# Optimization experiments

Measured on AMD Instinct MI355X. Metric: run time of the kernel, lower is better.

Reference implementation:

```python
import jax, jax.numpy as jnp
import numpy as np

GROUP_SIZE = 128


def setup_inputs() -> dict:
    key = jax.random.key(0)
    k1, k2, k3, k4, k5 = jax.random.split(key, 5)
    B, S, I, O = 4, 2048, 4096, 4096
    x = jax.random.normal(k1, (B, S, I), dtype=jnp.float32)
    logits = jax.random.normal(k2, (O, I, 3), dtype=jnp.float32)
    u = jax.random.uniform(k3, (O, I, 3), dtype=jnp.float32)
    scales = jax.random.uniform(k4, (O, I // GROUP_SIZE), dtype=jnp.float32)
    mask = jax.random.randint(k5, (O, I), 0, 2, dtype=jnp.int32)
    return {"x": x, "logits": logits, "u": u, "scales": scales, "mask": mask}


def reference(x, logits, u, scales, mask):
    # Gumbel noise: E ~ Exp(1) via inverse CDF, gumbel = -log(max(E, 1e-10))
    e = -jnp.log(jnp.clip(1.0 - u, 1e-12, 1.0))
    gumbels = -jnp.log(jnp.clip(e, 1e-10, None))
    # hard ternary sample (training path of TernaryReinMax.forward)
    samples = jnp.argmax(logits + gumbels, axis=-1)          # [O, I]
    one_hot = jax.nn.one_hot(samples, 3, dtype=jnp.float32)   # [O, I, 3]
    w = one_hot[..., 2] - one_hot[..., 0]                     # ternary {-1,0,1}
    O, I = w.shape
    G = GROUP_SIZE
    # per-group dequant scales along in_features, then mask
    w = (w.reshape(O, I // G, G) * scales[:, :, None]).reshape(O, I)
    w = w * mask.astype(w.dtype)
    # F.linear(x, w) = x @ w.T
    return jnp.einsum('bsi,oi->bso', x, w.astype(x.dtype))
```

## Files before the change

kernel.cpp:

```cpp
#include <hip/hip_runtime.h>
#include <hip/hip_bf16.h>

typedef unsigned short ushort_t;
typedef __attribute__((ext_vector_type(4))) float f32x4;
typedef __attribute__((ext_vector_type(8))) short short8;
typedef __attribute__((ext_vector_type(4))) unsigned short u16x4;
typedef __attribute__((ext_vector_type(8))) unsigned short u16x8;
typedef __attribute__((ext_vector_type(4))) int i32x4;

constexpr int Mdim = 8192;
constexpr int Ndim = 4096;
constexpr int Kdim = 4096;
constexpr int BM = 128, BN = 128, BK = 32;

__device__ __forceinline__ ushort_t f2bf(float f) {
  unsigned u = __float_as_uint(f);
  u += 0x7fffu + ((u >> 16) & 1u);
  return (ushort_t)(u >> 16);
}

__device__ __forceinline__ float gumbel_from_u(float u) {
  float e = -logf(fmaxf(1.0f - u, 1e-12f));
  return -logf(fmaxf(e, 1e-10f));
}

__global__ __launch_bounds__(256) void wgen_kernel(
    const f32x4* __restrict__ lg, const f32x4* __restrict__ uu,
    const float* __restrict__ scales, const i32x4* __restrict__ mask4,
    ushort_t* __restrict__ W) {
  int t = blockIdx.x * 256 + threadIdx.x;
  f32x4 L0 = lg[t * 3 + 0], L1 = lg[t * 3 + 1], L2 = lg[t * 3 + 2];
  f32x4 U0 = uu[t * 3 + 0], U1 = uu[t * 3 + 1], U2 = uu[t * 3 + 2];
  i32x4 mk = mask4[t];
  int idx = t << 2;
  int i = idx & (Kdim - 1);
  int o = idx >> 12;
  float sc = scales[(o << 5) | (i >> 7)];

  float lf[12], uf[12];
#pragma unroll
  for (int r = 0; r < 4; r++) { lf[r] = L0[r]; lf[4 + r] = L1[r]; lf[8 + r] = L2[r];
                                uf[r] = U0[r]; uf[4 + r] = U1[r]; uf[8 + r] = U2[r]; }
  u16x4 outv;
#pragma unroll
  for (int j = 0; j < 4; j++) {
    float s0 = lf[3 * j + 0] + gumbel_from_u(uf[3 * j + 0]);
    float s1 = lf[3 * j + 1] + gumbel_from_u(uf[3 * j + 1]);
    float s2 = lf[3 * j + 2] + gumbel_from_u(uf[3 * j + 2]);
    int a = 0; float b = s0;
    if (s1 > b) { b = s1; a = 1; }
    if (s2 > b) { b = s2; a = 2; }
    float wv = (a == 2) ? sc : ((a == 0) ? -sc : 0.0f);
    wv = mk[j] ? wv : 0.0f;
    outv[j] = f2bf(wv);
  }
  *reinterpret_cast<u16x4*>(W + idx) = outv;
}

__global__ __launch_bounds__(256) void xconv_kernel(
    const f32x4* __restrict__ x, u16x8* __restrict__ xb) {
  int t = blockIdx.x * 256 + threadIdx.x;
  f32x4 v0 = x[t * 2], v1 = x[t * 2 + 1];
  u16x8 p;
#pragma unroll
  for (int j = 0; j < 4; j++) { p[j] = f2bf(v0[j]); p[4 + j] = f2bf(v1[j]); }
  xb[t] = p;
}

#define GLOAD16(gp, lp)                                           \
  __builtin_amdgcn_global_load_lds(                               \
      (const __attribute__((address_space(1))) void*)(gp),        \
      (__attribute__((address_space(3))) void*)(lp), 16, 0, 0)

template <int AF32>
__global__ __launch_bounds__(256) void gemm_kernel(
    const ushort_t* __restrict__ Abf, const float* __restrict__ Af,
    const ushort_t* __restrict__ Bw, float* __restrict__ C) {
  __shared__ ushort_t As[BM * BK];
  __shared__ ushort_t Bs[BN * BK];

  const int tid = threadIdx.x;
  const int w = tid >> 6, l = tid & 63;

  int bid = blockIdx.x;
  const int nwg = gridDim.x;
  if ((nwg & 7) == 0) { const int cpx = nwg >> 3; bid = (bid & 7) * cpx + (bid >> 3); }
  const int tn = bid & (Ndim / BN - 1);
  const int tm = bid >> 5;

  const int wr = w >> 1, wc = w & 1;
  const int fr = l & 15, fq = l >> 4;

  f32x4 acc[4][4] = {};

  const int arow = w * 16 + (l >> 2);
  const int acol = (l & 3) * 8;
  const long abase = (long)(tm * BM) * Kdim;
  const long bbase = (long)(tn * BN) * Kdim;

  for (int kk = 0; kk < Kdim; kk += BK) {
    if constexpr (!AF32) {
#pragma unroll
      for (int s = 0; s < 2; s++) {
        const ushort_t* ga = Abf + abase + (long)(s * 64 + arow) * Kdim + kk + acol;
        GLOAD16(ga, &As[(s * 64 + w * 16) * BK]);
        const ushort_t* gb = Bw + bbase + (long)(s * 64 + arow) * Kdim + kk + acol;
        GLOAD16(gb, &Bs[(s * 64 + w * 16) * BK]);
      }
    } else {
#pragma unroll
      for (int s = 0; s < 2; s++) {
        const ushort_t* gb = Bw + bbase + (long)(s * 64 + arow) * Kdim + kk + acol;
        GLOAD16(gb, &Bs[(s * 64 + w * 16) * BK]);
      }
#pragma unroll
      for (int s = 0; s < 2; s++) {
        const int r2 = s * 64 + (tid >> 2);
        const int c2 = (tid & 3) * 8;
        const float* gx = Af + abase + (long)r2 * Kdim + kk + c2;
        f32x4 v0 = *reinterpret_cast<const f32x4*>(gx);
        f32x4 v1 = *reinterpret_cast<const f32x4*>(gx + 4);
        u16x8 pk;
#pragma unroll
        for (int j = 0; j < 4; j++) { pk[j] = f2bf(v0[j]); pk[4 + j] = f2bf(v1[j]); }
        *reinterpret_cast<u16x8*>(&As[r2 * BK + c2]) = pk;
      }
    }
    __syncthreads();

    short8 af[4], bfr[4];
#pragma unroll
    for (int i = 0; i < 4; i++)
      af[i] = *reinterpret_cast<const short8*>(&As[(wr * 64 + i * 16 + fr) * BK + fq * 8]);
#pragma unroll
    for (int i = 0; i < 4; i++)
      bfr[i] = *reinterpret_cast<const short8*>(&Bs[(wc * 64 + i * 16 + fr) * BK + fq * 8]);
#pragma unroll
    for (int i = 0; i < 4; i++)
#pragma unroll
      for (int j = 0; j < 4; j++)
        acc[i][j] = __builtin_amdgcn_mfma_f32_16x16x32_bf16(af[i], bfr[j], acc[i][j], 0, 0, 0);
    __syncthreads();
  }

  const long crow = (long)(tm * BM + wr * 64);
  const int ccol = tn * BN + wc * 64;
#pragma unroll
  for (int i = 0; i < 4; i++)
#pragma unroll
    for (int j = 0; j < 4; j++)
#pragma unroll
      for (int r = 0; r < 4; r++)
        C[(crow + i * 16 + fq * 4 + r) * (long)Ndim + ccol + j * 16 + fr] = acc[i][j][r];
}

extern "C" void kernel_launch(void* const* d_in, const int* in_sizes, int n_in,
                              void* d_out, int out_size, void* d_ws, size_t ws_size,
                              hipStream_t stream) {
  const float* x      = (const float*)d_in[0];
  const float* logits = (const float*)d_in[1];
  const float* u      = (const float*)d_in[2];
  const float* scales = (const float*)d_in[3];
  const int*   mask   = (const int*)d_in[4];
  float* out = (float*)d_out;

  ushort_t* W = (ushort_t*)d_ws;
  const size_t wbytes = (size_t)Ndim * Kdim * 2;
  const size_t xbytes = (size_t)Mdim * Kdim * 2;

  wgen_kernel<<<(Ndim * (long)Kdim / 4) / 256, 256, 0, stream>>>(
      (const f32x4*)logits, (const f32x4*)u, scales, (const i32x4*)mask, W);

  const int gblocks = (Mdim / BM) * (Ndim / BN);
  if (ws_size >= wbytes + xbytes) {
    ushort_t* xb = (ushort_t*)((char*)d_ws + wbytes);
    xconv_kernel<<<(Mdim * (long)Kdim / 8) / 256, 256, 0, stream>>>(
        (const f32x4*)x, (u16x8*)xb);
    gemm_kernel<0><<<gblocks, 256, 0, stream>>>(xb, nullptr, W, out);
  } else {
    gemm_kernel<1><<<gblocks, 256, 0, stream>>>(nullptr, x, W, out);
  }
}
```

Measured before the change: 949.1 us.

## Replace GEMM with 256x256 multi-stage pipelined LDS kernel and coalesce prep kernels

The main GEMM becomes a 512-thread kernel with 256x256 output tiles. It uses a 128KB swizzled LDS ring buffer filled by global_load_lds, with prefetch several stages ahead, explicit vmcnt waits, barriers and setprio around the MFMA blocks. This is meant to raise data reuse per tile and hide global-load latency that the old single-buffered 128x128 kernel exposed. The weight-generation kernel now stages logits and u through LDS for fully coalesced loads. The x-to-bf16 conversion kernel uses strided coalesced accesses. The hand-tuned wait counts and large LDS footprint limit occupancy to one block per CU and are fragile if the stage accounting is off.

```diff
diff --git a/kernel.cpp b/kernel.cpp
--- a/kernel.cpp
+++ b/kernel.cpp
@@ -11,7 +11,6 @@
 constexpr int Mdim = 8192;
 constexpr int Ndim = 4096;
 constexpr int Kdim = 4096;
-constexpr int BM = 128, BN = 128, BK = 32;
 
 __device__ __forceinline__ ushort_t f2bf(float f) {
   unsigned u = __float_as_uint(f);
@@ -25,28 +24,33 @@
 }
 
 __global__ __launch_bounds__(256) void wgen_kernel(
-    const f32x4* __restrict__ lg, const f32x4* __restrict__ uu,
+    const float* __restrict__ lg, const float* __restrict__ uu,
     const float* __restrict__ scales, const i32x4* __restrict__ mask4,
     ushort_t* __restrict__ W) {
-  int t = blockIdx.x * 256 + threadIdx.x;
-  f32x4 L0 = lg[t * 3 + 0], L1 = lg[t * 3 + 1], L2 = lg[t * 3 + 2];
-  f32x4 U0 = uu[t * 3 + 0], U1 = uu[t * 3 + 1], U2 = uu[t * 3 + 2];
-  i32x4 mk = mask4[t];
-  int idx = t << 2;
-  int i = idx & (Kdim - 1);
-  int o = idx >> 12;
-  float sc = scales[(o << 5) | (i >> 7)];
-
-  float lf[12], uf[12];
-#pragma unroll
-  for (int r = 0; r < 4; r++) { lf[r] = L0[r]; lf[4 + r] = L1[r]; lf[8 + r] = L2[r];
-                                uf[r] = U0[r]; uf[4 + r] = U1[r]; uf[8 + r] = U2[r]; }
+  __shared__ float ls[3072];
+  __shared__ float us_[3072];
+  const int tid = threadIdx.x;
+  const f32x4* gl = (const f32x4*)lg + (size_t)blockIdx.x * 768;
+  const f32x4* gu = (const f32x4*)uu + (size_t)blockIdx.x * 768;
+#pragma unroll
+  for (int w = 0; w < 3; w++) {
+    ((f32x4*)ls)[w * 256 + tid]  = gl[w * 256 + tid];
+    ((f32x4*)us_)[w * 256 + tid] = gu[w * 256 + tid];
+  }
+  i32x4 mk = mask4[(size_t)blockIdx.x * 256 + tid];
+  __syncthreads();
+  const long idx = (long)blockIdx.x * 1024 + tid * 4;
+  const int i = (int)(idx & (Kdim - 1));
+  const int o = (int)(idx >> 12);
+  const float sc = scales[(o << 5) | (i >> 7)];
   u16x4 outv;
 #pragma unroll
   for (int j = 0; j < 4; j++) {
-    float s0 = lf[3 * j + 0] + gumbel_from_u(uf[3 * j + 0]);
-    float s1 = lf[3 * j + 1] + gumbel_from_u(uf[3 * j + 1]);
-    float s2 = lf[3 * j + 2] + gumbel_from_u(uf[3 * j + 2]);
+    const float* lp = &ls[tid * 12 + j * 3];
+    const float* up = &us_[tid * 12 + j * 3];
+    float s0 = lp[0] + gumbel_from_u(up[0]);
+    float s1 = lp[1] + gumbel_from_u(up[1]);
+    float s2 = lp[2] + gumbel_from_u(up[2]);
     int a = 0; float b = s0;
     if (s1 > b) { b = s1; a = 1; }
     if (s2 > b) { b = s2; a = 2; }
@@ -58,13 +62,15 @@
 }
 
 __global__ __launch_bounds__(256) void xconv_kernel(
-    const f32x4* __restrict__ x, u16x8* __restrict__ xb) {
-  int t = blockIdx.x * 256 + threadIdx.x;
-  f32x4 v0 = x[t * 2], v1 = x[t * 2 + 1];
-  u16x8 p;
-#pragma unroll
-  for (int j = 0; j < 4; j++) { p[j] = f2bf(v0[j]); p[4 + j] = f2bf(v1[j]); }
-  xb[t] = p;
+    const f32x4* __restrict__ x, u16x4* __restrict__ xb) {
+  const size_t base = (size_t)blockIdx.x * 512;
+  const int tid = threadIdx.x;
+  f32x4 v0 = x[base + tid], v1 = x[base + 256 + tid];
+  u16x4 p0, p1;
+#pragma unroll
+  for (int j = 0; j < 4; j++) { p0[j] = f2bf(v0[j]); p1[j] = f2bf(v1[j]); }
+  xb[base + tid] = p0;
+  xb[base + 256 + tid] = p1;
 }
 
 #define GLOAD16(gp, lp)                                           \
@@ -72,62 +78,140 @@
       (const __attribute__((address_space(1))) void*)(gp),        \
       (__attribute__((address_space(3))) void*)(lp), 16, 0, 0)
 
-template <int AF32>
-__global__ __launch_bounds__(256) void gemm_kernel(
-    const ushort_t* __restrict__ Abf, const float* __restrict__ Af,
-    const ushort_t* __restrict__ Bw, float* __restrict__ C) {
+__global__ __launch_bounds__(512, 2) void gemm8_kernel(
+    const ushort_t* __restrict__ Abf, const ushort_t* __restrict__ Bw,
+    float* __restrict__ C) {
+  __shared__ char lds[131072];
+
+  const int tid = threadIdx.x;
+  const int wv = tid >> 6, l = tid & 63;
+  const int fr = l & 15, fq = l >> 4;
+  const int wr = wv >> 2, wc = wv & 3;
+
+  int bid = blockIdx.x;
+  bid = (bid & 7) * 64 + (bid >> 3);
+  const int tn = bid & 15, tm = bid >> 4;
+
+  const char* baseA[2];
+  const char* baseB[2];
+#pragma unroll
+  for (int w = 0; w < 2; w++) {
+    int q = (w * 512 + tid) * 16;
+    int a = q ^ (((q >> 6) & 3) << 4);
+    int r = a >> 6, cb = a & 63;
+    baseA[w] = (const char*)Abf + (size_t)(tm * 256 + r) * (Kdim * 2) + cb;
+    baseB[w] = (const char*)Bw  + (size_t)(tn * 256 + r) * (Kdim * 2) + cb;
+  }
+  const int wvoff = wv * 1024;
+
+  auto stage_j = [&](int j) {
+    int s = j & 3;
+    int colb = (j >> 2) * 128 + ((s >> 1) << 6);
+    int o0 = __builtin_amdgcn_readfirstlane((j & 7) * 16384 + wvoff);
+    const char* b0 = (s & 1) ? baseB[0] : baseA[0];
+    const char* b1 = (s & 1) ? baseB[1] : baseA[1];
+    GLOAD16(b0 + colb, lds + o0);
+    GLOAD16(b1 + colb, lds + o0 + 8192);
+  };
+
+  const int Xsw = (fr & 3) << 4;
+  const int aA0 = ((wr * 128 + fr) * 64 + fq * 16) ^ Xsw;
+  const int aB0 = ((wc * 64 + fr) * 64 + fq * 16) ^ Xsw;
+
+  f32x4 acc[8][4] = {};
+
+  for (int j = 0; j < 5; ++j) stage_j(j);
+  asm volatile("s_waitcnt vmcnt(6)" ::: "memory");
+  __builtin_amdgcn_s_barrier();
+
+  for (int t = 0; t < 64; ++t) {
+    const int b = t & 1;
+#pragma unroll
+    for (int p = 0; p < 4; ++p) {
+      const int ks = p >> 1, mh = p & 1;
+      const char* As_ = lds + (b * 4 + ks * 2) * 16384;
+      const char* Bs_ = lds + (b * 4 + ks * 2 + 1) * 16384;
+      short8 af[4], bv[4];
+#pragma unroll
+      for (int i = 0; i < 4; ++i)
+        af[i] = *reinterpret_cast<const short8*>(As_ + (aA0 + mh * 4096 + i * 1024));
+#pragma unroll
+      for (int i = 0; i < 4; ++i)
+        bv[i] = *reinterpret_cast<const short8*>(Bs_ + (aB0 + i * 1024));
+      const int jst = 4 * t + p + 5;
+      if (jst < 256) stage_j(jst);
+      __builtin_amdgcn_s_barrier();
+      asm volatile("s_waitcnt lgkmcnt(0)" ::: "memory");
+      __builtin_amdgcn_sched_barrier(0);
+      __builtin_amdgcn_s_setprio(1);
+#pragma unroll
+      for (int i = 0; i < 4; ++i)
+#pragma unroll
+        for (int j2 = 0; j2 < 4; ++j2)
+          acc[mh * 4 + i][j2] = __builtin_amdgcn_mfma_f32_16x16x32_bf16(
+              af[i], bv[j2], acc[mh * 4 + i][j2], 0, 0, 0);
+      __builtin_amdgcn_s_setprio(0);
+      __builtin_amdgcn_sched_barrier(0);
+      if (p == 1) {
+        if (t < 63) asm volatile("s_waitcnt vmcnt(6)" ::: "memory");
+        else        asm volatile("s_waitcnt vmcnt(0)" ::: "memory");
+      } else if (p == 3) {
+        if (t < 62)       asm volatile("s_waitcnt vmcnt(6)" ::: "memory");
+        else if (t == 62) asm volatile("s_waitcnt vmcnt(4)" ::: "memory");
+      }
+      __builtin_amdgcn_s_barrier();
+    }
+  }
+
+  float* Cw = C + (size_t)(tm * 256 + wr * 128) * Ndim + tn * 256 + wc * 64;
+#pragma unroll
+  for (int mi = 0; mi < 8; ++mi)
+#pragma unroll
+    for (int nj = 0; nj < 4; ++nj)
+#pragma unroll
+      for (int r = 0; r < 4; ++r)
+        Cw[(size_t)(mi * 16 + fq * 4 + r) * Ndim + nj * 16 + fr] = acc[mi][nj][r];
+}
+
+__global__ __launch_bounds__(256) void gemm_fb(
+    const float* __restrict__ Af, const ushort_t* __restrict__ Bw,
+    float* __restrict__ C) {
+  constexpr int BM = 128, BN = 128, BK = 32;
   __shared__ ushort_t As[BM * BK];
   __shared__ ushort_t Bs[BN * BK];
-
   const int tid = threadIdx.x;
   const int w = tid >> 6, l = tid & 63;
-
   int bid = blockIdx.x;
   const int nwg = gridDim.x;
   if ((nwg & 7) == 0) { const int cpx = nwg >> 3; bid = (bid & 7) * cpx + (bid >> 3); }
   const int tn = bid & (Ndim / BN - 1);
   const int tm = bid >> 5;
-
   const int wr = w >> 1, wc = w & 1;
   const int fr = l & 15, fq = l >> 4;
-
   f32x4 acc[4][4] = {};
-
   const int arow = w * 16 + (l >> 2);
   const int acol = (l & 3) * 8;
   const long abase = (long)(tm * BM) * Kdim;
   const long bbase = (long)(tn * BN) * Kdim;
-
   for (int kk = 0; kk < Kdim; kk += BK) {
-    if constexpr (!AF32) {
-#pragma unroll
-      for (int s = 0; s < 2; s++) {
-        const ushort_t* ga = Abf + abase + (long)(s * 64 + arow) * Kdim + kk + acol;
-        GLOAD16(ga, &As[(s * 64 + w * 16) * BK]);
-        const ushort_t* gb = Bw + bbase + (long)(s * 64 + arow) * Kdim + kk + acol;
-        GLOAD16(gb, &Bs[(s * 64 + w * 16) * BK]);
-      }
-    } else {
-#pragma unroll
-      for (int s = 0; s < 2; s++) {
-        const ushort_t* gb = Bw + bbase + (long)(s * 64 + arow) * Kdim + kk + acol;
-        GLOAD16(gb, &Bs[(s * 64 + w * 16) * BK]);
-      }
-#pragma unroll
-      for (int s = 0; s < 2; s++) {
-        const int r2 = s * 64 + (tid >> 2);
-        const int c2 = (tid & 3) * 8;
-        const float* gx = Af + abase + (long)r2 * Kdim + kk + c2;
-        f32x4 v0 = *reinterpret_cast<const f32x4*>(gx);
-        f32x4 v1 = *reinterpret_cast<const f32x4*>(gx + 4);
-        u16x8 pk;
-#pragma unroll
-        for (int j = 0; j < 4; j++) { pk[j] = f2bf(v0[j]); pk[4 + j] = f2bf(v1[j]); }
-        *reinterpret_cast<u16x8*>(&As[r2 * BK + c2]) = pk;
-      }
+#pragma unroll
+    for (int s = 0; s < 2; s++) {
+      const ushort_t* gb = Bw + bbase + (long)(s * 64 + arow) * Kdim + kk + acol;
+      GLOAD16(gb, &Bs[(s * 64 + w * 16) * BK]);
+    }
+#pragma unroll
+    for (int s = 0; s < 2; s++) {
+      const int r2 = s * 64 + (tid >> 2);
+      const int c2 = (tid & 3) * 8;
+      const float* gx = Af + abase + (long)r2 * Kdim + kk + c2;
+      f32x4 v0 = *reinterpret_cast<const f32x4*>(gx);
+      f32x4 v1 = *reinterpret_cast<const f32x4*>(gx + 4);
+      u16x8 pk;
+#pragma unroll
+      for (int j = 0; j < 4; j++) { pk[j] = f2bf(v0[j]); pk[4 + j] = f2bf(v1[j]); }
+      *reinterpret_cast<u16x8*>(&As[r2 * BK + c2]) = pk;
     }
     __syncthreads();
-
     short8 af[4], bfr[4];
 #pragma unroll
     for (int i = 0; i < 4; i++)
@@ -142,7 +226,6 @@
         acc[i][j] = __builtin_amdgcn_mfma_f32_16x16x32_bf16(af[i], bfr[j], acc[i][j], 0, 0, 0);
     __syncthreads();
   }
-
   const long crow = (long)(tm * BM + wr * 64);
   const int ccol = tn * BN + wc * 64;
 #pragma unroll
@@ -168,16 +251,15 @@
   const size_t wbytes = (size_t)Ndim * Kdim * 2;
   const size_t xbytes = (size_t)Mdim * Kdim * 2;
 
-  wgen_kernel<<<(Ndim * (long)Kdim / 4) / 256, 256, 0, stream>>>(
-      (const f32x4*)logits, (const f32x4*)u, scales, (const i32x4*)mask, W);
-
-  const int gblocks = (Mdim / BM) * (Ndim / BN);
+  wgen_kernel<<<(Ndim * (long)Kdim) / 1024, 256, 0, stream>>>(
+      logits, u, scales, (const i32x4*)mask, W);
+
   if (ws_size >= wbytes + xbytes) {
     ushort_t* xb = (ushort_t*)((char*)d_ws + wbytes);
-    xconv_kernel<<<(Mdim * (long)Kdim / 8) / 256, 256, 0, stream>>>(
-        (const f32x4*)x, (u16x8*)xb);
-    gemm_kernel<0><<<gblocks, 256, 0, stream>>>(xb, nullptr, W, out);
+    xconv_kernel<<<(Mdim * (long)Kdim / 4) / 512, 256, 0, stream>>>(
+        (const f32x4*)x, (u16x4*)xb);
+    gemm8_kernel<<<(Mdim / 256) * (Ndim / 256), 512, 0, stream>>>(xb, W, out);
   } else {
-    gemm_kernel<1><<<gblocks, 256, 0, stream>>>(nullptr, x, W, out);
-  }
-}
+    gemm_fb<<<(Mdim / 128) * (Ndim / 128), 256, 0, stream>>>(x, W, out);
+  }
+}
```

New measurement: 794.1 us. 1.2x faster.
